# Kernel tuning notes

Measured on AMD Instinct MI355X. Metric: run time of the kernel, lower is better.

The kernel has to match this reference:

```python
import jax, jax.numpy as jnp
import numpy as np

NUM_CLASSES = 6625
FEAT_DIM = 2048
BATCH = 4096


def setup_inputs() -> dict:
    key = jax.random.key(0)
    k1, k2, k3 = jax.random.split(key, 3)
    x = jax.random.normal(k1, (BATCH, FEAT_DIM), dtype=jnp.float32)
    labels = jax.random.randint(k2, (BATCH,), 0, NUM_CLASSES, dtype=jnp.int64)
    centers = jax.random.normal(k3, (NUM_CLASSES, FEAT_DIM), dtype=jnp.float32)
    return {"x": x, "labels": labels, "centers": centers}


def reference(x, labels, centers):
    # Original builds a dense [B, C] squared-distance matrix and then, per row i,
    # keeps only the entry at column labels[i], clamps, and averages.
    # Mathematically that kept entry is:
    #   ||x_i||^2 + ||c_{y_i}||^2 - 2 * <x_i, c_{y_i}>
    # so we gather the labeled center and compute the same value directly.
    c = centers[labels]                                   # [B, D]
    x_sq = jnp.sum(x * x, axis=1)                         # [B]
    c_sq = jnp.sum(c * c, axis=1)                         # [B]
    cross = jnp.einsum('bd,bd->b', x, c)                  # [B]
    dist = x_sq + c_sq - 2.0 * cross                      # [B]
    dist = jnp.clip(dist, 1e-12, 1e12)
    return jnp.mean(dist)
```

## Files before the change

kernel.cpp:

```cpp
#include <hip/hip_runtime.h>

#define BATCH 4096
#define FEAT_DIM 2048
#define NTHREADS 256
#define ROWS_PER_BLOCK 4
#define NBLOCKS (BATCH / ROWS_PER_BLOCK)

__global__ __launch_bounds__(NTHREADS) void cl_rows(
        const float* __restrict__ x,
        const int* __restrict__ labels,
        const float* __restrict__ centers,
        float* __restrict__ partial) {
    const int tid  = threadIdx.x;
    const int wave = tid >> 6;
    const int lane = tid & 63;
    const int row  = blockIdx.x * ROWS_PER_BLOCK + wave;

    const int lab = labels[row];
    const float4* __restrict__ xr =
        reinterpret_cast<const float4*>(x + (size_t)row * FEAT_DIM);
    const float4* __restrict__ cr =
        reinterpret_cast<const float4*>(centers + (size_t)lab * FEAT_DIM);

    float4 a[8], b[8];
    #pragma unroll
    for (int k = 0; k < 8; ++k) a[k] = xr[lane + 64 * k];
    #pragma unroll
    for (int k = 0; k < 8; ++k) b[k] = cr[lane + 64 * k];

    float s = 0.f;
    #pragma unroll
    for (int k = 0; k < 8; ++k) {
        float dx = a[k].x - b[k].x;
        float dy = a[k].y - b[k].y;
        float dz = a[k].z - b[k].z;
        float dw = a[k].w - b[k].w;
        s += dx * dx + dy * dy + dz * dz + dw * dw;
    }

    #pragma unroll
    for (int off = 32; off > 0; off >>= 1) s += __shfl_down(s, off, 64);

    __shared__ float sw[ROWS_PER_BLOCK];
    if (lane == 0) {
        sw[wave] = fminf(fmaxf(s, 1e-12f), 1e12f);
    }
    __syncthreads();

    if (tid == 0) {
        float t = 0.f;
        #pragma unroll
        for (int w = 0; w < ROWS_PER_BLOCK; ++w) t += sw[w];
        partial[blockIdx.x] = t;
    }
}

__global__ __launch_bounds__(NTHREADS) void cl_final(
        const float* __restrict__ partial,
        float* __restrict__ out) {
    const int tid = threadIdx.x;
    float s = 0.f;
    #pragma unroll
    for (int i = tid; i < NBLOCKS; i += NTHREADS) s += partial[i];

    #pragma unroll
    for (int off = 32; off > 0; off >>= 1) s += __shfl_down(s, off, 64);

    __shared__ float sw[NTHREADS / 64];
    if ((tid & 63) == 0) sw[tid >> 6] = s;
    __syncthreads();

    if (tid == 0) {
        float t = 0.f;
        #pragma unroll
        for (int w = 0; w < NTHREADS / 64; ++w) t += sw[w];
        out[0] = t * (1.0f / BATCH);
    }
}

extern "C" void kernel_launch(void* const* d_in, const int* in_sizes, int n_in,
                              void* d_out, int out_size, void* d_ws, size_t ws_size,
                              hipStream_t stream) {
    const float* x       = (const float*)d_in[0];
    const int*   labels  = (const int*)d_in[1];
    const float* centers = (const float*)d_in[2];
    float*       out     = (float*)d_out;
    float*       partial = (float*)d_ws;

    cl_rows<<<NBLOCKS, NTHREADS, 0, stream>>>(x, labels, centers, partial);
    cl_final<<<1, NTHREADS, 0, stream>>>(partial, out);
}
```

Measured before the change: 17.93 us.

## Fuse final reduction into row kernel using last-block atomic counter

```diff
diff --git a/kernel.cpp b/kernel.cpp
--- a/kernel.cpp
+++ b/kernel.cpp
@@ -6,15 +6,18 @@
 #define ROWS_PER_BLOCK 4
 #define NBLOCKS (BATCH / ROWS_PER_BLOCK)
 
-__global__ __launch_bounds__(NTHREADS) void cl_rows(
+__global__ __launch_bounds__(NTHREADS) void cl_fused(
         const float* __restrict__ x,
         const int* __restrict__ labels,
         const float* __restrict__ centers,
-        float* __restrict__ partial) {
+        float* __restrict__ partial,
+        unsigned int* __restrict__ counter,
+        float* __restrict__ out) {
     const int tid  = threadIdx.x;
     const int wave = tid >> 6;
     const int lane = tid & 63;
-    const int row  = blockIdx.x * ROWS_PER_BLOCK + wave;
+    const int bid  = blockIdx.x;
+    const int row  = bid * ROWS_PER_BLOCK + wave;
 
     const int lab = labels[row];
     const float4* __restrict__ xr =
@@ -42,39 +45,38 @@
     for (int off = 32; off > 0; off >>= 1) s += __shfl_down(s, off, 64);
 
     __shared__ float sw[ROWS_PER_BLOCK];
-    if (lane == 0) {
-        sw[wave] = fminf(fmaxf(s, 1e-12f), 1e12f);
+    __shared__ int is_winner;
+    if (lane == 0) sw[wave] = fminf(fmaxf(s, 1e-12f), 1e12f);
+    __syncthreads();
+
+    if (tid == 0) {
+        float t = sw[0] + sw[1] + sw[2] + sw[3];
+        partial[bid] = t;
+        __threadfence();
+        unsigned int old = atomicAdd(counter, 1u);
+        is_winner = ((old & (NBLOCKS - 1)) == (NBLOCKS - 1)) ? 1 : 0;
     }
     __syncthreads();
 
-    if (tid == 0) {
-        float t = 0.f;
+    if (is_winner) {
+        __threadfence();
+        float acc = 0.f;
         #pragma unroll
-        for (int w = 0; w < ROWS_PER_BLOCK; ++w) t += sw[w];
-        partial[blockIdx.x] = t;
-    }
-}
+        for (int i = tid; i < NBLOCKS; i += NTHREADS) acc += partial[i];
 
-__global__ __launch_bounds__(NTHREADS) void cl_final(
-        const float* __restrict__ partial,
-        float* __restrict__ out) {
-    const int tid = threadIdx.x;
-    float s = 0.f;
-    #pragma unroll
-    for (int i = tid; i < NBLOCKS; i += NTHREADS) s += partial[i];
+        #pragma unroll
+        for (int off = 32; off > 0; off >>= 1) acc += __shfl_down(acc, off, 64);
 
-    #pragma unroll
-    for (int off = 32; off > 0; off >>= 1) s += __shfl_down(s, off, 64);
+        __shared__ float fw[NTHREADS / 64];
+        if ((tid & 63) == 0) fw[tid >> 6] = acc;
+        __syncthreads();
 
-    __shared__ float sw[NTHREADS / 64];
-    if ((tid & 63) == 0) sw[tid >> 6] = s;
-    __syncthreads();
-
-    if (tid == 0) {
-        float t = 0.f;
-        #pragma unroll
-        for (int w = 0; w < NTHREADS / 64; ++w) t += sw[w];
-        out[0] = t * (1.0f / BATCH);
+        if (tid == 0) {
+            float total = 0.f;
+            #pragma unroll
+            for (int w = 0; w < NTHREADS / 64; ++w) total += fw[w];
+            out[0] = total * (1.0f / BATCH);
+        }
     }
 }
 
@@ -85,8 +87,10 @@
     const int*   labels  = (const int*)d_in[1];
     const float* centers = (const float*)d_in[2];
     float*       out     = (float*)d_out;
-    float*       partial = (float*)d_ws;
 
-    cl_rows<<<NBLOCKS, NTHREADS, 0, stream>>>(x, labels, centers, partial);
-    cl_final<<<1, NTHREADS, 0, stream>>>(partial, out);
+    unsigned int* counter = (unsigned int*)d_ws;
+    float*        partial = (float*)((char*)d_ws + 4096);
+
+    cl_fused<<<NBLOCKS, NTHREADS, 0, stream>>>(x, labels, centers,
+                                               partial, counter, out);
 }
```

Result: slower. 45.36 us (+153.1%).
